# Optimization experiments

Hardware: AMD Instinct MI355X
Metric: run time of the kernel (lower is better)

Reference implementation:

```python
import jax, jax.numpy as jnp
import numpy as np

N_NODES = 50000
N_EDGES = 800000
DIM = 256
DEPTH = 4
N_REL = 4
EPS = 1e-5


def setup_inputs() -> dict:
    key = jax.random.key(0)
    ks = jax.random.split(key, 8)
    scale = 1.0 / np.sqrt(DIM)
    return {
        "node_embedding": jax.random.normal(ks[0], (N_NODES, DIM), jnp.float32),
        "weights": jax.random.normal(ks[1], (DEPTH, N_REL, DIM, DIM), jnp.float32) * scale,
        "roots": jax.random.normal(ks[2], (DEPTH, DIM, DIM), jnp.float32) * scale,
        "biases": jax.random.normal(ks[3], (DEPTH, DIM), jnp.float32) * 0.01,
        "ln_gamma": jnp.ones((DEPTH, DIM), jnp.float32),
        "ln_beta": jnp.zeros((DEPTH, DIM), jnp.float32),
        "edge_index": jax.random.randint(ks[4], (2, N_EDGES), 0, N_NODES, jnp.int32),
        "edge_type": jax.random.randint(ks[5], (N_EDGES,), 0, N_REL, jnp.int32),
    }


def _rgcn_layer(X, W, root, bias, gamma, beta, src, dst, etype, inv_deg):
    # RGCNConv with aggr='mean': per-relation transform, then per-relation mean
    # over incoming edges at the target node, summed across relations.
    h = jnp.einsum('ni,rio->rno', X, W)            # [R, N, D]
    msg = h[etype, src] * inv_deg[:, None]         # [E, D] gather + per-relation 1/deg
    agg = jax.ops.segment_sum(msg, dst, num_segments=X.shape[0])  # [N, D]
    out = agg + X @ root + bias
    # LayerNorm
    mu = jnp.mean(out, axis=-1, keepdims=True)
    var = jnp.mean(jnp.square(out - mu), axis=-1, keepdims=True)
    out = (out - mu) * jax.lax.rsqrt(var + EPS) * gamma + beta
    out = jax.nn.elu(out)
    return out + X  # residual connection (dropout p=0 -> identity)


def reference(node_embedding, weights, roots, biases, ln_gamma, ln_beta, edge_index, edge_type):
    src, dst = edge_index[0], edge_index[1]
    # per-(node, relation) in-degree for the relation-wise mean aggregation
    cnt = jnp.zeros((node_embedding.shape[0], N_REL), node_embedding.dtype)
    cnt = cnt.at[dst, edge_type].add(1.0)
    inv_deg = 1.0 / jnp.maximum(cnt[dst, edge_type], 1.0)  # [E]
    X = node_embedding
    for l in range(DEPTH):
        X = _rgcn_layer(X, weights[l], roots[l], biases[l], ln_gamma[l], ln_beta[l],
                        src, dst, edge_type, inv_deg)
    return X
```

## Files before the change

### kernel.cpp

```cpp
#include <hip/hip_runtime.h>
#include <hip/hip_bf16.h>
#include <stdint.h>

#define NN 50000
#define NE 800000
#define DD 256
#define NL 4
#define NRL 4
#define KT 1280
#define KA 1024
#define NMT 782
#define MTB 131072
#define NTILE 40

typedef float f32x4 __attribute__((ext_vector_type(4)));
typedef __bf16 bf16x8 __attribute__((ext_vector_type(8)));
typedef __bf16 bf16x4 __attribute__((ext_vector_type(4)));
typedef unsigned short u16x4 __attribute__((ext_vector_type(4)));

static __device__ __forceinline__ unsigned short f2bf(float f) {
  __bf16 h = (__bf16)f;
  return __builtin_bit_cast(unsigned short, h);
}

static __device__ __forceinline__ u16x4 pk4(f32x4 v) {
  u16x4 o;
  o.x = f2bf(v.x); o.y = f2bf(v.y); o.z = f2bf(v.z); o.w = f2bf(v.w);
  return o;
}

static __device__ __forceinline__ void async16(const void* g, void* l) {
  __builtin_amdgcn_global_load_lds(
      (const __attribute__((address_space(1))) unsigned int*)g,
      (__attribute__((address_space(3))) unsigned int*)l, 16, 0, 0);
}


__global__ __launch_bounds__(256) void k_hist(const int* __restrict__ ei,
                                              const int* __restrict__ et,
                                              int* __restrict__ cntNR) {
  int e = blockIdx.x * 256 + threadIdx.x;
  if (e >= NE) return;
  int dst = ei[NE + e];
  int r = et[e];
  atomicAdd(&cntNR[dst * 4 + r], 1);
}

__global__ __launch_bounds__(256) void k_scan1(const int* __restrict__ cntNR,
                                               int* __restrict__ offs,
                                               int* __restrict__ bsum) {
  __shared__ int sd[256];
  const int t = threadIdx.x;
  const int n = blockIdx.x * 256 + t;
  int deg = 0;
  if (n < NN) {
    const int* c = cntNR + n * 4;
    deg = c[0] + c[1] + c[2] + c[3];
  }
  sd[t] = deg;
  __syncthreads();
  int val = deg;
  for (int d = 1; d < 256; d <<= 1) {
    int other = (t >= d) ? sd[t - d] : 0;
    __syncthreads();
    val += other;
    sd[t] = val;
    __syncthreads();
  }
  if (n < NN) offs[n] = val - deg;
  if (t == 255) bsum[blockIdx.x] = val;
}

__global__ __launch_bounds__(256) void k_scan2(const int* __restrict__ bsum,
                                               int* __restrict__ boff, int nb) {
  __shared__ int sd[256];
  const int t = threadIdx.x;
  int v = (t < nb) ? bsum[t] : 0;
  sd[t] = v;
  __syncthreads();
  int val = v;
  for (int d = 1; d < 256; d <<= 1) {
    int other = (t >= d) ? sd[t - d] : 0;
    __syncthreads();
    val += other;
    sd[t] = val;
    __syncthreads();
  }
  boff[t] = val - v;
}

__global__ __launch_bounds__(256) void k_scan3(int* __restrict__ offs,
                                               const int* __restrict__ boff,
                                               int* __restrict__ cursor) {
  int n = blockIdx.x * 256 + threadIdx.x;
  if (n < NN) {
    int o = offs[n] + boff[blockIdx.x];
    offs[n] = o;
    cursor[n] = o;
  }
  if (n == 0) offs[NN] = NE;
}

__global__ __launch_bounds__(256) void k_scatter(const int* __restrict__ ei,
                                                 const int* __restrict__ et,
                                                 int* __restrict__ cursor,
                                                 uint32_t* __restrict__ packed) {
  int e = blockIdx.x * 256 + threadIdx.x;
  if (e >= NE) return;
  int src = ei[e];
  int dst = ei[NE + e];
  int r = et[e];
  int pos = atomicAdd(&cursor[dst], 1);
  packed[pos] = (uint32_t)src | ((uint32_t)r << 16);
}

__global__ __launch_bounds__(256) void k_wconv(const float* __restrict__ weights,
                                               const float* __restrict__ roots,
                                               __hip_bfloat16* __restrict__ WbigT) {
  int idx = blockIdx.x * 256 + threadIdx.x;
  if (idx >= NL * DD * KT) return;
  int l = idx / 327680;
  int rem = idx - l * 327680;
  int kt = rem / 8192;
  int rem2 = rem - kt * 8192;
  int row = rem2 >> 5;
  int q = rem2 & 31;
  int s = q >> 3, e = q & 7;
  int k = kt * 32 + ((s ^ ((row >> 1) & 3)) << 3) + e;
  float v;
  if (k < KA) {
    int r = k >> 8, i = k & 255;
    v = weights[(((size_t)(l * NRL + r) * DD) + i) * DD + row];
  } else {
    int i = k - KA;
    v = roots[((size_t)l * DD + i) * DD + row];
  }
  WbigT[idx] = __float2bfloat16(v);
}

__global__ __launch_bounds__(256) void k_cast(const float* __restrict__ X,
                                              __hip_bfloat16* __restrict__ Xbf) {
  int i = blockIdx.x * 256 + threadIdx.x;
  if (i >= NN * 64) return;
  const f32x4* Xv = (const f32x4*)X;
  ((u16x4*)Xbf)[i] = pk4(Xv[i]);
}


__global__ __launch_bounds__(256) void k_agg(const __hip_bfloat16* __restrict__ Xbf,
                                             const uint32_t* __restrict__ packed,
                                             const int* __restrict__ offs,
                                             const int* __restrict__ cntNR,
                                             __hip_bfloat16* __restrict__ Abig) {
  const int wid = (blockIdx.x * 256 + threadIdx.x) >> 6;
  const int lane = threadIdx.x & 63;
  if (wid >= NN) return;
  const int beg = offs[wid];
  const int end = offs[wid + 1];
  const bf16x4* __restrict__ Xv = (const bf16x4*)Xbf;

  f32x4 a0 = {0.f, 0.f, 0.f, 0.f}, a1 = a0, a2 = a0, a3 = a0;

  for (int e = beg; e < end; e += 8) {
    uint32_t pv[8];
    bf16x4 vv[8];
#pragma unroll
    for (int i = 0; i < 8; ++i) {
      int ee = e + i;
      ee = (ee < end) ? ee : (end - 1);
      pv[i] = packed[ee];
    }
#pragma unroll
    for (int i = 0; i < 8; ++i) {
      vv[i] = Xv[(int)(pv[i] & 0xFFFFu) * 64 + lane];
    }
    const int nv = end - e;
#pragma unroll
    for (int i = 0; i < 8; ++i) {
      if (i < nv) {
        int r = (int)(pv[i] >> 16);
        f32x4 v = {(float)vv[i][0], (float)vv[i][1], (float)vv[i][2], (float)vv[i][3]};
        if (r == 0) a0 += v;
        else if (r == 1) a1 += v;
        else if (r == 2) a2 += v;
        else a3 += v;
      }
    }
  }

  const int* c = cntNR + wid * 4;
  int c0 = c[0], c1 = c[1], c2 = c[2], c3 = c[3];
  float s0 = 1.0f / (float)(c0 > 1 ? c0 : 1);
  float s1 = 1.0f / (float)(c1 > 1 ? c1 : 1);
  float s2 = 1.0f / (float)(c2 > 1 ? c2 : 1);
  float s3 = 1.0f / (float)(c3 > 1 ? c3 : 1);

  {
    const int row = wid & 63;
    const int fsw = (row >> 1) & 3;
    char* Ab = (char*)Abig + (size_t)(wid >> 6) * MTB + (size_t)(lane >> 3) * 4096 +
               row * 64 + ((((lane >> 1) & 3) ^ fsw) << 4) + (lane & 1) * 8;
    *(u16x4*)(Ab + 0 * 32768) = pk4(a0 * s0);
    *(u16x4*)(Ab + 1 * 32768) = pk4(a1 * s1);
    *(u16x4*)(Ab + 2 * 32768) = pk4(a2 * s2);
    *(u16x4*)(Ab + 3 * 32768) = pk4(a3 * s3);
  }
}


#define GBUF 20480
#define EPAD 260

__global__ __launch_bounds__(256, 2) void k_gemm(const __hip_bfloat16* __restrict__ A,
                                                 const __hip_bfloat16* __restrict__ Xbf_in,
                                                 const __hip_bfloat16* __restrict__ Bt,
                                                 const float* __restrict__ bias,
                                                 const float* __restrict__ gamma,
                                                 const float* __restrict__ beta,
                                                 const float* __restrict__ Xin,
                                                 float* __restrict__ Xout,
                                                 __hip_bfloat16* __restrict__ Xbf_out) {
  __shared__ __align__(16) char sLDS[4 * GBUF];
  float(*LDSf)[EPAD] = (float(*)[EPAD])sLDS;
  float(*sRed)[4] = (float(*)[4])(sLDS + 69632);

  const int tid = threadIdx.x;
  const int w = tid >> 6;
  const int lane = tid & 63;
  const int wm = w >> 1, wn = w & 1;
  const int quad = lane >> 4, l15 = lane & 15;
  const int mBase = blockIdx.x * 64;

  const int srow = lane >> 2;
  const int kc = (lane & 3) ^ ((srow >> 1) & 3);
  int am = mBase + w * 16 + srow;
  if (am >= NN) am = NN - 1;
  const char* agx = (const char*)Xbf_in + (size_t)am * (DD * 2) + kc * 16;

  const char* agp = (const char*)A + (size_t)blockIdx.x * MTB + w * 1024 + lane * 16;
  const char* bgp = (const char*)Bt + w * 4096 + lane * 16;

  char* const lA = sLDS + w * 1024;
  char* const lB = sLDS + 4096 + w * 4096;

  f32x4 acc[2][8];
#pragma unroll
  for (int i = 0; i < 2; ++i)
#pragma unroll
    for (int j = 0; j < 8; ++j) acc[i][j] = (f32x4){0.f, 0.f, 0.f, 0.f};

  const int aslot = (quad ^ ((l15 >> 1) & 3)) * 16;
  const char* const aBase = sLDS + (wm * 32 + l15) * 64 + aslot;
  const char* const bBase = sLDS + 4096 + (wn * 128 + l15) * 64 + aslot;

  auto STAGE = [&](int buf, int ts) {
    char* la = lA + buf * GBUF;
    char* lb = lB + buf * GBUF;
    if (ts < 32) {
      async16(agp + (size_t)ts * 4096, la);
    } else {
      async16(agx + (ts - 32) * 64, la);
    }
    const char* bt = bgp + (size_t)ts * 16384;
    async16(bt, lb);
    async16(bt + 1024, lb + 1024);
    async16(bt + 2048, lb + 2048);
    async16(bt + 3072, lb + 3072);
  };

  auto COMPUTE = [&](int buf) {
    const char* aAddr = aBase + buf * GBUF;
    const char* bAddr = bBase + buf * GBUF;
    bf16x8 a0 = *(const bf16x8*)(aAddr + 0 * 1024);
    bf16x8 a1 = *(const bf16x8*)(aAddr + 1 * 1024);
#pragma unroll
    for (int nt = 0; nt < 8; ++nt) {
      bf16x8 b = *(const bf16x8*)(bAddr + nt * 1024);
      acc[0][nt] = __builtin_amdgcn_mfma_f32_16x16x32_bf16(a0, b, acc[0][nt], 0, 0, 0);
      acc[1][nt] = __builtin_amdgcn_mfma_f32_16x16x32_bf16(a1, b, acc[1][nt], 0, 0, 0);
    }
  };

  STAGE(0, 0);
  STAGE(1, 1);
  int cb = 0, sb = 2;
  for (int t = 0; t < NTILE - 2; ++t) {
    STAGE(sb, t + 2);
    __builtin_amdgcn_sched_barrier(0);
    asm volatile("s_waitcnt vmcnt(10)" ::: "memory");
    __builtin_amdgcn_s_barrier();
    __builtin_amdgcn_sched_barrier(0);
    COMPUTE(cb);
    cb = (cb + 1) & 3;
    sb = (sb + 1) & 3;
  }
  asm volatile("s_waitcnt vmcnt(5)" ::: "memory");
  __builtin_amdgcn_s_barrier();
  __builtin_amdgcn_sched_barrier(0);
  COMPUTE(cb);
  cb = (cb + 1) & 3;
  asm volatile("s_waitcnt vmcnt(0)" ::: "memory");
  __builtin_amdgcn_s_barrier();
  __builtin_amdgcn_sched_barrier(0);
  COMPUTE(cb);

  __syncthreads();

  float bv[8], gv[8], bev[8];
#pragma unroll
  for (int nt = 0; nt < 8; ++nt) {
    int n = wn * 128 + nt * 16 + l15;
    bv[nt] = bias[n];
    gv[nt] = gamma[n];
    bev[nt] = beta[n];
  }

#pragma unroll
  for (int mt = 0; mt < 2; ++mt) {
#pragma unroll
    for (int reg = 0; reg < 4; ++reg) {
      float s = 0.f, q = 0.f;
#pragma unroll
      for (int nt = 0; nt < 8; ++nt) {
        float v = acc[mt][nt][reg] + bv[nt];
        acc[mt][nt][reg] = v;
        s += v;
        q += v * v;
      }
#pragma unroll
      for (int d = 1; d < 16; d <<= 1) {
        s += __shfl_xor(s, d, 64);
        q += __shfl_xor(q, d, 64);
      }
      if (l15 == 0) {
        int row = wm * 32 + mt * 16 + quad * 4 + reg;
        sRed[row][wn * 2] = s;
        sRed[row][wn * 2 + 1] = q;
      }
    }
  }
  __syncthreads();

#pragma unroll
  for (int mt = 0; mt < 2; ++mt) {
#pragma unroll
    for (int reg = 0; reg < 4; ++reg) {
      int row = wm * 32 + mt * 16 + quad * 4 + reg;
      float ts = sRed[row][0] + sRed[row][2];
      float tq = sRed[row][1] + sRed[row][3];
      float mean = ts * (1.0f / 256.0f);
      float var = tq * (1.0f / 256.0f) - mean * mean;
      float rstd = rsqrtf(var + 1e-5f);
#pragma unroll
      for (int nt = 0; nt < 8; ++nt) {
        float v = (acc[mt][nt][reg] - mean) * rstd * gv[nt] + bev[nt];
        v = v > 0.0f ? v : (__expf(v) - 1.0f);
        LDSf[row][wn * 128 + nt * 16 + l15] = v;
      }
    }
  }
  __syncthreads();

#pragma unroll
  for (int rr = 0; rr < 16; ++rr) {
    const int row = w * 16 + rr;
    const int m = mBase + row;
    if (m < NN) {
      f32x4 v = *(const f32x4*)&LDSf[row][lane * 4];
      f32x4 xi = __builtin_nontemporal_load((const f32x4*)(Xin + (size_t)m * 256 + lane * 4));
      f32x4 res = v + xi;
      __builtin_nontemporal_store(res, (f32x4*)(Xout + (size_t)m * 256 + lane * 4));
      *(u16x4*)(Xbf_out + (size_t)m * 256 + lane * 4) = pk4(res);
    }
  }
}


extern "C" void kernel_launch(void* const* d_in, const int* in_sizes, int n_in,
                              void* d_out, int out_size, void* d_ws, size_t ws_size,
                              hipStream_t stream) {
  const float* X0 = (const float*)d_in[0];
  const float* weights = (const float*)d_in[1];
  const float* roots = (const float*)d_in[2];
  const float* biases = (const float*)d_in[3];
  const float* ln_g = (const float*)d_in[4];
  const float* ln_b = (const float*)d_in[5];
  const int* eidx = (const int*)d_in[6];
  const int* etyp = (const int*)d_in[7];
  float* out = (float*)d_out;

  char* ws = (char*)d_ws;
  size_t off = 0;
  auto alloc = [&](size_t bytes) -> char* {
    char* p = ws + off;
    off = (off + bytes + 255) & ~(size_t)255;
    return p;
  };
  __hip_bfloat16* Abig = (__hip_bfloat16*)alloc((size_t)NMT * MTB);
  __hip_bfloat16* WbigT = (__hip_bfloat16*)alloc((size_t)NL * DD * KT * 2);
  float* Xb0 = (float*)alloc((size_t)NN * DD * 4);
  float* Xb1 = (float*)alloc((size_t)NN * DD * 4);
  __hip_bfloat16* Xbf0 = (__hip_bfloat16*)alloc((size_t)NN * DD * 2);
  __hip_bfloat16* Xbf1 = (__hip_bfloat16*)alloc((size_t)NN * DD * 2);
  int* cntNR = (int*)alloc((size_t)NN * 4 * 4);
  int* offs = (int*)alloc((size_t)(NN + 1) * 4);
  int* cursor = (int*)alloc((size_t)NN * 4);
  uint32_t* packed = (uint32_t*)alloc((size_t)NE * 4);
  int* bsum = (int*)alloc(256 * 4);
  int* boff = (int*)alloc(256 * 4);
  (void)ws_size; (void)in_sizes; (void)n_in; (void)out_size;

  (void)hipMemsetAsync(cntNR, 0, (size_t)NN * 16, stream);
  (void)hipMemsetAsync((char*)Abig + (size_t)(NMT - 1) * MTB, 0, MTB, stream);
  k_hist<<<(NE + 255) / 256, 256, 0, stream>>>(eidx, etyp, cntNR);
  const int NB = (NN + 255) / 256;
  k_scan1<<<NB, 256, 0, stream>>>(cntNR, offs, bsum);
  k_scan2<<<1, 256, 0, stream>>>(bsum, boff, NB);
  k_scan3<<<NB, 256, 0, stream>>>(offs, boff, cursor);
  k_scatter<<<(NE + 255) / 256, 256, 0, stream>>>(eidx, etyp, cursor, packed);
  k_wconv<<<(NL * DD * KT + 255) / 256, 256, 0, stream>>>(weights, roots, WbigT);
  k_cast<<<(NN * 64 + 255) / 256, 256, 0, stream>>>(X0, Xbf0);

  const float* Xin = X0;
  for (int l = 0; l < NL; ++l) {
    float* Xout = (l == NL - 1) ? out : ((l & 1) ? Xb1 : Xb0);
    const __hip_bfloat16* Xbin = (l & 1) ? Xbf1 : Xbf0;
    __hip_bfloat16* Xbout = (l & 1) ? Xbf0 : Xbf1;
    k_agg<<<(NN * 64 + 255) / 256, 256, 0, stream>>>(Xbin, packed, offs, cntNR, Abig);
    k_gemm<<<(NN + 63) / 64, 256, 0, stream>>>(Abig, Xbin,
                                               WbigT + (size_t)l * DD * KT,
                                               biases + (size_t)l * DD,
                                               ln_g + (size_t)l * DD,
                                               ln_b + (size_t)l * DD, Xin, Xout, Xbout);
    Xin = Xout;
  }
}
```

Before: 800.7 us.

## Fuse edge aggregation into GEMM kernel with relation-sorted CSR

Removes the separate aggregation kernel and its global A buffer. Each GEMM block now gathers neighbor features per relation straight into LDS, then runs the MFMA K-tiles for that relation while weight tiles stream in with a 3-buffer async pipeline. Edges are now sorted by (dst, relation) using per-relation cursors, so the relation branch disappears from the inner loop. This cuts the global write and read of the aggregated activations, but the irregular gathers now sit inside the GEMM blocks, with less latency hiding and per-relation barriers.

```diff
diff --git a/kernel.cpp b/kernel.cpp
--- a/kernel.cpp
+++ b/kernel.cpp
@@ -10,7 +10,6 @@
 #define KT 1280
 #define KA 1024
 #define NMT 782
-#define MTB 131072
 #define NTILE 40
 
 typedef float f32x4 __attribute__((ext_vector_type(4)));
@@ -91,27 +90,32 @@
 
 __global__ __launch_bounds__(256) void k_scan3(int* __restrict__ offs,
                                                const int* __restrict__ boff,
-                                               int* __restrict__ cursor) {
+                                               const int* __restrict__ cntNR,
+                                               int* __restrict__ cursor4) {
   int n = blockIdx.x * 256 + threadIdx.x;
   if (n < NN) {
     int o = offs[n] + boff[blockIdx.x];
     offs[n] = o;
-    cursor[n] = o;
+    const int4 c = *(const int4*)(cntNR + n * 4);
+    cursor4[n * 4 + 0] = o;
+    cursor4[n * 4 + 1] = o + c.x;
+    cursor4[n * 4 + 2] = o + c.x + c.y;
+    cursor4[n * 4 + 3] = o + c.x + c.y + c.z;
   }
   if (n == 0) offs[NN] = NE;
 }
 
 __global__ __launch_bounds__(256) void k_scatter(const int* __restrict__ ei,
                                                  const int* __restrict__ et,
-                                                 int* __restrict__ cursor,
+                                                 int* __restrict__ cursor4,
                                                  uint32_t* __restrict__ packed) {
   int e = blockIdx.x * 256 + threadIdx.x;
   if (e >= NE) return;
   int src = ei[e];
   int dst = ei[NE + e];
   int r = et[e];
-  int pos = atomicAdd(&cursor[dst], 1);
-  packed[pos] = (uint32_t)src | ((uint32_t)r << 16);
+  int pos = atomicAdd(&cursor4[dst * 4 + r], 1);
+  packed[pos] = (uint32_t)src;
 }
 
 __global__ __launch_bounds__(256) void k_wconv(const float* __restrict__ weights,
@@ -147,72 +151,10 @@
 }
 
 
-__global__ __launch_bounds__(256) void k_agg(const __hip_bfloat16* __restrict__ Xbf,
-                                             const uint32_t* __restrict__ packed,
-                                             const int* __restrict__ offs,
-                                             const int* __restrict__ cntNR,
-                                             __hip_bfloat16* __restrict__ Abig) {
-  const int wid = (blockIdx.x * 256 + threadIdx.x) >> 6;
-  const int lane = threadIdx.x & 63;
-  if (wid >= NN) return;
-  const int beg = offs[wid];
-  const int end = offs[wid + 1];
-  const bf16x4* __restrict__ Xv = (const bf16x4*)Xbf;
-
-  f32x4 a0 = {0.f, 0.f, 0.f, 0.f}, a1 = a0, a2 = a0, a3 = a0;
-
-  for (int e = beg; e < end; e += 8) {
-    uint32_t pv[8];
-    bf16x4 vv[8];
-#pragma unroll
-    for (int i = 0; i < 8; ++i) {
-      int ee = e + i;
-      ee = (ee < end) ? ee : (end - 1);
-      pv[i] = packed[ee];
-    }
-#pragma unroll
-    for (int i = 0; i < 8; ++i) {
-      vv[i] = Xv[(int)(pv[i] & 0xFFFFu) * 64 + lane];
-    }
-    const int nv = end - e;
-#pragma unroll
-    for (int i = 0; i < 8; ++i) {
-      if (i < nv) {
-        int r = (int)(pv[i] >> 16);
-        f32x4 v = {(float)vv[i][0], (float)vv[i][1], (float)vv[i][2], (float)vv[i][3]};
-        if (r == 0) a0 += v;
-        else if (r == 1) a1 += v;
-        else if (r == 2) a2 += v;
-        else a3 += v;
-      }
-    }
-  }
-
-  const int* c = cntNR + wid * 4;
-  int c0 = c[0], c1 = c[1], c2 = c[2], c3 = c[3];
-  float s0 = 1.0f / (float)(c0 > 1 ? c0 : 1);
-  float s1 = 1.0f / (float)(c1 > 1 ? c1 : 1);
-  float s2 = 1.0f / (float)(c2 > 1 ? c2 : 1);
-  float s3 = 1.0f / (float)(c3 > 1 ? c3 : 1);
-
-  {
-    const int row = wid & 63;
-    const int fsw = (row >> 1) & 3;
-    char* Ab = (char*)Abig + (size_t)(wid >> 6) * MTB + (size_t)(lane >> 3) * 4096 +
-               row * 64 + ((((lane >> 1) & 3) ^ fsw) << 4) + (lane & 1) * 8;
-    *(u16x4*)(Ab + 0 * 32768) = pk4(a0 * s0);
-    *(u16x4*)(Ab + 1 * 32768) = pk4(a1 * s1);
-    *(u16x4*)(Ab + 2 * 32768) = pk4(a2 * s2);
-    *(u16x4*)(Ab + 3 * 32768) = pk4(a3 * s3);
-  }
-}
-
-
-#define GBUF 20480
-#define EPAD 260
-
-__global__ __launch_bounds__(256, 2) void k_gemm(const __hip_bfloat16* __restrict__ A,
-                                                 const __hip_bfloat16* __restrict__ Xbf_in,
+__global__ __launch_bounds__(256, 2) void k_rgcn(const __hip_bfloat16* __restrict__ Xbf_in,
+                                                 const uint32_t* __restrict__ packed,
+                                                 const int* __restrict__ offs,
+                                                 const int* __restrict__ cntNR,
                                                  const __hip_bfloat16* __restrict__ Bt,
                                                  const float* __restrict__ bias,
                                                  const float* __restrict__ gamma,
@@ -220,7 +162,8 @@
                                                  const float* __restrict__ Xin,
                                                  float* __restrict__ Xout,
                                                  __hip_bfloat16* __restrict__ Xbf_out) {
-  __shared__ __align__(16) char sLDS[4 * GBUF];
+  __shared__ __align__(16) char sLDS[81920];
+#define EPAD 260
   float(*LDSf)[EPAD] = (float(*)[EPAD])sLDS;
   float(*sRed)[4] = (float(*)[4])(sLDS + 69632);
 
@@ -231,36 +174,22 @@
   const int quad = lane >> 4, l15 = lane & 15;
   const int mBase = blockIdx.x * 64;
 
-  const int srow = lane >> 2;
-  const int kc = (lane & 3) ^ ((srow >> 1) & 3);
-  int am = mBase + w * 16 + srow;
-  if (am >= NN) am = NN - 1;
-  const char* agx = (const char*)Xbf_in + (size_t)am * (DD * 2) + kc * 16;
-
-  const char* agp = (const char*)A + (size_t)blockIdx.x * MTB + w * 1024 + lane * 16;
   const char* bgp = (const char*)Bt + w * 4096 + lane * 16;
-
-  char* const lA = sLDS + w * 1024;
-  char* const lB = sLDS + 4096 + w * 4096;
-
-  f32x4 acc[2][8];
-#pragma unroll
-  for (int i = 0; i < 2; ++i)
-#pragma unroll
-    for (int j = 0; j < 8; ++j) acc[i][j] = (f32x4){0.f, 0.f, 0.f, 0.f};
 
   const int aslot = (quad ^ ((l15 >> 1) & 3)) * 16;
   const char* const aBase = sLDS + (wm * 32 + l15) * 64 + aslot;
-  const char* const bBase = sLDS + 4096 + (wn * 128 + l15) * 64 + aslot;
-
-  auto STAGE = [&](int buf, int ts) {
-    char* la = lA + buf * GBUF;
-    char* lb = lB + buf * GBUF;
-    if (ts < 32) {
-      async16(agp + (size_t)ts * 4096, la);
-    } else {
-      async16(agx + (ts - 32) * 64, la);
-    }
+  const char* const bBase = sLDS + 32768 + (wn * 128 + l15) * 64 + aslot;
+
+  const bf16x4* __restrict__ Xv = (const bf16x4*)Xbf_in;
+
+  f32x4 acc[2][8];
+#pragma unroll
+  for (int i = 0; i < 2; ++i)
+#pragma unroll
+    for (int j = 0; j < 8; ++j) acc[i][j] = (f32x4){0.f, 0.f, 0.f, 0.f};
+
+  auto STAGE_B = [&](int buf, int ts) {
+    char* lb = sLDS + 32768 + buf * 16384 + w * 4096;
     const char* bt = bgp + (size_t)ts * 16384;
     async16(bt, lb);
     async16(bt + 1024, lb + 1024);
@@ -268,11 +197,11 @@
     async16(bt + 3072, lb + 3072);
   };
 
-  auto COMPUTE = [&](int buf) {
-    const char* aAddr = aBase + buf * GBUF;
-    const char* bAddr = bBase + buf * GBUF;
-    bf16x8 a0 = *(const bf16x8*)(aAddr + 0 * 1024);
-    bf16x8 a1 = *(const bf16x8*)(aAddr + 1 * 1024);
+  auto COMPUTE = [&](int t8, int bb) {
+    const char* aAddr = aBase + t8 * 4096;
+    const char* bAddr = bBase + bb * 16384;
+    bf16x8 a0 = *(const bf16x8*)(aAddr);
+    bf16x8 a1 = *(const bf16x8*)(aAddr + 1024);
 #pragma unroll
     for (int nt = 0; nt < 8; ++nt) {
       bf16x8 b = *(const bf16x8*)(bAddr + nt * 1024);
@@ -281,29 +210,91 @@
     }
   };
 
-  STAGE(0, 0);
-  STAGE(1, 1);
-  int cb = 0, sb = 2;
-  for (int t = 0; t < NTILE - 2; ++t) {
-    STAGE(sb, t + 2);
-    __builtin_amdgcn_sched_barrier(0);
-    asm volatile("s_waitcnt vmcnt(10)" ::: "memory");
-    __builtin_amdgcn_s_barrier();
-    __builtin_amdgcn_sched_barrier(0);
-    COMPUTE(cb);
-    cb = (cb + 1) & 3;
-    sb = (sb + 1) & 3;
-  }
-  asm volatile("s_waitcnt vmcnt(5)" ::: "memory");
-  __builtin_amdgcn_s_barrier();
-  __builtin_amdgcn_sched_barrier(0);
-  COMPUTE(cb);
-  cb = (cb + 1) & 3;
-  asm volatile("s_waitcnt vmcnt(0)" ::: "memory");
-  __builtin_amdgcn_s_barrier();
-  __builtin_amdgcn_sched_barrier(0);
-  COMPUTE(cb);
-
+  auto AGG = [&](int r) {
+    for (int rr = 0; rr < 16; ++rr) {
+      const int row = w * 16 + rr;
+      int n = mBase + row;
+      if (n >= NN) n = NN - 1;
+      const int4 c = *(const int4*)(cntNR + n * 4);
+      int beg = offs[n];
+      int cr;
+      if (r == 0) { cr = c.x; }
+      else if (r == 1) { beg += c.x; cr = c.y; }
+      else if (r == 2) { beg += c.x + c.y; cr = c.z; }
+      else { beg += c.x + c.y + c.z; cr = c.w; }
+      const int end = beg + cr;
+      f32x4 a = {0.f, 0.f, 0.f, 0.f};
+      for (int e = beg; e < end; e += 4) {
+        uint32_t pv[4];
+        bf16x4 vv[4];
+#pragma unroll
+        for (int i = 0; i < 4; ++i) {
+          int ee = e + i;
+          ee = (ee < end) ? ee : (end - 1);
+          pv[i] = packed[ee];
+        }
+#pragma unroll
+        for (int i = 0; i < 4; ++i) vv[i] = Xv[(int)pv[i] * 64 + lane];
+        const int nv = end - e;
+#pragma unroll
+        for (int i = 0; i < 4; ++i) {
+          if (i < nv) {
+            a.x += (float)vv[i][0];
+            a.y += (float)vv[i][1];
+            a.z += (float)vv[i][2];
+            a.w += (float)vv[i][3];
+          }
+        }
+      }
+      const float s = 1.0f / (float)(cr > 1 ? cr : 1);
+      const int fsw = (row >> 1) & 3;
+      char* dst = sLDS + (size_t)(lane >> 3) * 4096 + row * 64 +
+                  ((((lane >> 1) & 3) ^ fsw) << 4) + (lane & 1) * 8;
+      *(u16x4*)dst = pk4(a * s);
+    }
+  };
+
+  auto ROOT = [&]() {
+    for (int rr = 0; rr < 16; ++rr) {
+      const int row = w * 16 + rr;
+      int n = mBase + row;
+      if (n >= NN) n = NN - 1;
+      bf16x4 v = Xv[n * 64 + lane];
+      const int fsw = (row >> 1) & 3;
+      char* dst = sLDS + (size_t)(lane >> 3) * 4096 + row * 64 +
+                  ((((lane >> 1) & 3) ^ fsw) << 4) + (lane & 1) * 8;
+      *(bf16x4*)dst = v;
+    }
+  };
+
+  STAGE_B(0, 0);
+  STAGE_B(1, 1);
+
+  int bb = 0;
+  for (int r = 0; r < 5; ++r) {
+    if (r) {
+      __builtin_amdgcn_sched_barrier(0);
+      __builtin_amdgcn_s_barrier();
+      __builtin_amdgcn_sched_barrier(0);
+    }
+    if (r < 4) AGG(r); else ROOT();
+    __syncthreads();
+#pragma unroll
+    for (int t8 = 0; t8 < 8; ++t8) {
+      const int t = r * 8 + t8;
+      if (r == 4 && t8 == 7) {
+        asm volatile("s_waitcnt vmcnt(0)" ::: "memory");
+      } else {
+        asm volatile("s_waitcnt vmcnt(4)" ::: "memory");
+      }
+      __builtin_amdgcn_s_barrier();
+      __builtin_amdgcn_sched_barrier(0);
+      if (t + 2 < 40) STAGE_B((bb + 2 == 3) ? 0 : ((bb + 2 == 4) ? 1 : bb + 2), t + 2);
+      __builtin_amdgcn_sched_barrier(0);
+      COMPUTE(t8, bb);
+      bb = (bb == 2) ? 0 : bb + 1;
+    }
+  }
   __syncthreads();
 
   float bv[8], gv[8], bev[8];
@@ -396,7 +387,6 @@
     off = (off + bytes + 255) & ~(size_t)255;
     return p;
   };
-  __hip_bfloat16* Abig = (__hip_bfloat16*)alloc((size_t)NMT * MTB);
   __hip_bfloat16* WbigT = (__hip_bfloat16*)alloc((size_t)NL * DD * KT * 2);
   float* Xb0 = (float*)alloc((size_t)NN * DD * 4);
   float* Xb1 = (float*)alloc((size_t)NN * DD * 4);
@@ -404,20 +394,19 @@
   __hip_bfloat16* Xbf1 = (__hip_bfloat16*)alloc((size_t)NN * DD * 2);
   int* cntNR = (int*)alloc((size_t)NN * 4 * 4);
   int* offs = (int*)alloc((size_t)(NN + 1) * 4);
-  int* cursor = (int*)alloc((size_t)NN * 4);
+  int* cursor4 = (int*)alloc((size_t)NN * 4 * 4);
   uint32_t* packed = (uint32_t*)alloc((size_t)NE * 4);
   int* bsum = (int*)alloc(256 * 4);
   int* boff = (int*)alloc(256 * 4);
   (void)ws_size; (void)in_sizes; (void)n_in; (void)out_size;
 
   (void)hipMemsetAsync(cntNR, 0, (size_t)NN * 16, stream);
-  (void)hipMemsetAsync((char*)Abig + (size_t)(NMT - 1) * MTB, 0, MTB, stream);
   k_hist<<<(NE + 255) / 256, 256, 0, stream>>>(eidx, etyp, cntNR);
   const int NB = (NN + 255) / 256;
   k_scan1<<<NB, 256, 0, stream>>>(cntNR, offs, bsum);
   k_scan2<<<1, 256, 0, stream>>>(bsum, boff, NB);
-  k_scan3<<<NB, 256, 0, stream>>>(offs, boff, cursor);
-  k_scatter<<<(NE + 255) / 256, 256, 0, stream>>>(eidx, etyp, cursor, packed);
+  k_scan3<<<NB, 256, 0, stream>>>(offs, boff, cntNR, cursor4);
+  k_scatter<<<(NE + 255) / 256, 256, 0, stream>>>(eidx, etyp, cursor4, packed);
   k_wconv<<<(NL * DD * KT + 255) / 256, 256, 0, stream>>>(weights, roots, WbigT);
   k_cast<<<(NN * 64 + 255) / 256, 256, 0, stream>>>(X0, Xbf0);
 
@@ -426,12 +415,11 @@
     float* Xout = (l == NL - 1) ? out : ((l & 1) ? Xb1 : Xb0);
     const __hip_bfloat16* Xbin = (l & 1) ? Xbf1 : Xbf0;
     __hip_bfloat16* Xbout = (l & 1) ? Xbf0 : Xbf1;
-    k_agg<<<(NN * 64 + 255) / 256, 256, 0, stream>>>(Xbin, packed, offs, cntNR, Abig);
-    k_gemm<<<(NN + 63) / 64, 256, 0, stream>>>(Abig, Xbin,
-                                               WbigT + (size_t)l * DD * KT,
-                                               biases + (size_t)l * DD,
-                                               ln_g + (size_t)l * DD,
-                                               ln_b + (size_t)l * DD, Xin, Xout, Xbout);
+    k_rgcn<<<NMT, 256, 0, stream>>>(Xbin, packed, offs, cntNR,
+                                    WbigT + (size_t)l * DD * KT,
+                                    biases + (size_t)l * DD,
+                                    ln_g + (size_t)l * DD,
+                                    ln_b + (size_t)l * DD, Xin, Xout, Xbout);
     Xin = Xout;
   }
 }
```

After: 1.427 ms. +78.2%, slower.

## Bucket CSR edges by relation and gather 16-byte rows with half-wave split

Applied to the files above, without the earlier changes.

The CSR build now keeps a cursor per (node, relation), so each node's edges come out grouped by relation and the relation bits no longer need to be packed into the edge word. The aggregation kernel then walks each relation bucket separately, so the per-edge relation branching goes away. Each half-wave gathers a different edge with 16-byte bf16x8 loads, and the two halves are combined with a cross-lane shuffle. Results are written as 16-byte nontemporal stores, at the cost of more serial loop passes per node (four buckets) and masked wasted loads when bucket sizes are not multiples of four.

```diff
diff --git a/kernel.cpp b/kernel.cpp
--- a/kernel.cpp
+++ b/kernel.cpp
@@ -17,6 +17,7 @@
 typedef __bf16 bf16x8 __attribute__((ext_vector_type(8)));
 typedef __bf16 bf16x4 __attribute__((ext_vector_type(4)));
 typedef unsigned short u16x4 __attribute__((ext_vector_type(4)));
+typedef unsigned short u16x8 __attribute__((ext_vector_type(8)));
 
 static __device__ __forceinline__ unsigned short f2bf(float f) {
   __bf16 h = (__bf16)f;
@@ -26,6 +27,13 @@
 static __device__ __forceinline__ u16x4 pk4(f32x4 v) {
   u16x4 o;
   o.x = f2bf(v.x); o.y = f2bf(v.y); o.z = f2bf(v.z); o.w = f2bf(v.w);
+  return o;
+}
+
+static __device__ __forceinline__ u16x8 pk8(f32x4 lo, f32x4 hi) {
+  u16x8 o;
+  o[0] = f2bf(lo.x); o[1] = f2bf(lo.y); o[2] = f2bf(lo.z); o[3] = f2bf(lo.w);
+  o[4] = f2bf(hi.x); o[5] = f2bf(hi.y); o[6] = f2bf(hi.z); o[7] = f2bf(hi.w);
   return o;
 }
 
@@ -91,27 +99,32 @@
 
 __global__ __launch_bounds__(256) void k_scan3(int* __restrict__ offs,
                                                const int* __restrict__ boff,
-                                               int* __restrict__ cursor) {
+                                               const int* __restrict__ cntNR,
+                                               int* __restrict__ cursor4) {
   int n = blockIdx.x * 256 + threadIdx.x;
   if (n < NN) {
     int o = offs[n] + boff[blockIdx.x];
     offs[n] = o;
-    cursor[n] = o;
+    const int4 c = *(const int4*)(cntNR + n * 4);
+    cursor4[n * 4 + 0] = o;
+    cursor4[n * 4 + 1] = o + c.x;
+    cursor4[n * 4 + 2] = o + c.x + c.y;
+    cursor4[n * 4 + 3] = o + c.x + c.y + c.z;
   }
   if (n == 0) offs[NN] = NE;
 }
 
 __global__ __launch_bounds__(256) void k_scatter(const int* __restrict__ ei,
                                                  const int* __restrict__ et,
-                                                 int* __restrict__ cursor,
+                                                 int* __restrict__ cursor4,
                                                  uint32_t* __restrict__ packed) {
   int e = blockIdx.x * 256 + threadIdx.x;
   if (e >= NE) return;
   int src = ei[e];
   int dst = ei[NE + e];
   int r = et[e];
-  int pos = atomicAdd(&cursor[dst], 1);
-  packed[pos] = (uint32_t)src | ((uint32_t)r << 16);
+  int pos = atomicAdd(&cursor4[dst * 4 + r], 1);
+  packed[pos] = (uint32_t)src;
 }
 
 __global__ __launch_bounds__(256) void k_wconv(const float* __restrict__ weights,
@@ -155,55 +168,57 @@
   const int wid = (blockIdx.x * 256 + threadIdx.x) >> 6;
   const int lane = threadIdx.x & 63;
   if (wid >= NN) return;
-  const int beg = offs[wid];
-  const int end = offs[wid + 1];
-  const bf16x4* __restrict__ Xv = (const bf16x4*)Xbf;
-
-  f32x4 a0 = {0.f, 0.f, 0.f, 0.f}, a1 = a0, a2 = a0, a3 = a0;
-
-  for (int e = beg; e < end; e += 8) {
-    uint32_t pv[8];
-    bf16x4 vv[8];
-#pragma unroll
-    for (int i = 0; i < 8; ++i) {
-      int ee = e + i;
-      ee = (ee < end) ? ee : (end - 1);
-      pv[i] = packed[ee];
-    }
-#pragma unroll
-    for (int i = 0; i < 8; ++i) {
-      vv[i] = Xv[(int)(pv[i] & 0xFFFFu) * 64 + lane];
-    }
-    const int nv = end - e;
-#pragma unroll
-    for (int i = 0; i < 8; ++i) {
-      if (i < nv) {
-        int r = (int)(pv[i] >> 16);
-        f32x4 v = {(float)vv[i][0], (float)vv[i][1], (float)vv[i][2], (float)vv[i][3]};
-        if (r == 0) a0 += v;
-        else if (r == 1) a1 += v;
-        else if (r == 2) a2 += v;
-        else a3 += v;
-      }
-    }
-  }
-
-  const int* c = cntNR + wid * 4;
-  int c0 = c[0], c1 = c[1], c2 = c[2], c3 = c[3];
-  float s0 = 1.0f / (float)(c0 > 1 ? c0 : 1);
-  float s1 = 1.0f / (float)(c1 > 1 ? c1 : 1);
-  float s2 = 1.0f / (float)(c2 > 1 ? c2 : 1);
-  float s3 = 1.0f / (float)(c3 > 1 ? c3 : 1);
-
-  {
-    const int row = wid & 63;
-    const int fsw = (row >> 1) & 3;
-    char* Ab = (char*)Abig + (size_t)(wid >> 6) * MTB + (size_t)(lane >> 3) * 4096 +
-               row * 64 + ((((lane >> 1) & 3) ^ fsw) << 4) + (lane & 1) * 8;
-    *(u16x4*)(Ab + 0 * 32768) = pk4(a0 * s0);
-    *(u16x4*)(Ab + 1 * 32768) = pk4(a1 * s1);
-    *(u16x4*)(Ab + 2 * 32768) = pk4(a2 * s2);
-    *(u16x4*)(Ab + 3 * 32768) = pk4(a3 * s3);
+  const int g = lane >> 5;
+  const int j = lane & 31;
+  const bf16x8* __restrict__ Xv8 = (const bf16x8*)Xbf;
+
+  const int4 c = *(const int4*)(cntNR + wid * 4);
+  const int crArr[4] = {c.x, c.y, c.z, c.w};
+  int s = offs[wid];
+
+  const int row = wid & 63;
+  const int fsw = (row >> 1) & 3;
+  char* const Ab = (char*)Abig + (size_t)(wid >> 6) * MTB + row * 64 +
+                   (((j & 3) ^ fsw) << 4);
+
+#pragma unroll
+  for (int r = 0; r < 4; ++r) {
+    const int cr = crArr[r];
+    const int end = s + cr;
+    f32x4 aLo = {0.f, 0.f, 0.f, 0.f}, aHi = aLo;
+    for (int e = s; e < end; e += 4) {
+      int e0 = e + g;
+      int e1 = e + 2 + g;
+      const float m0 = (e0 < end) ? 1.f : 0.f;
+      const float m1 = (e1 < end) ? 1.f : 0.f;
+      e0 = (e0 < end) ? e0 : end - 1;
+      e1 = (e1 < end) ? e1 : end - 1;
+      const uint32_t p0 = packed[e0];
+      const uint32_t p1 = packed[e1];
+      const bf16x8 x0 = Xv8[(int)p0 * 32 + j];
+      const bf16x8 x1 = Xv8[(int)p1 * 32 + j];
+#pragma unroll
+      for (int k2 = 0; k2 < 4; ++k2) {
+        aLo[k2] += (float)x0[k2] * m0;
+        aHi[k2] += (float)x0[4 + k2] * m0;
+      }
+#pragma unroll
+      for (int k2 = 0; k2 < 4; ++k2) {
+        aLo[k2] += (float)x1[k2] * m1;
+        aHi[k2] += (float)x1[4 + k2] * m1;
+      }
+    }
+#pragma unroll
+    for (int k2 = 0; k2 < 4; ++k2) {
+      aLo[k2] += __shfl_xor(aLo[k2], 32, 64);
+      aHi[k2] += __shfl_xor(aHi[k2], 32, 64);
+    }
+    const float sc = 1.0f / (float)(cr > 1 ? cr : 1);
+    if (g == 0) {
+      __builtin_nontemporal_store(pk8(aLo * sc, aHi * sc),
+                                  (u16x8*)(Ab + (size_t)(r * 8 + (j >> 2)) * 4096));
+    }
+    s = end;
   }
 }
 
@@ -404,7 +419,7 @@
   __hip_bfloat16* Xbf1 = (__hip_bfloat16*)alloc((size_t)NN * DD * 2);
   int* cntNR = (int*)alloc((size_t)NN * 4 * 4);
   int* offs = (int*)alloc((size_t)(NN + 1) * 4);
-  int* cursor = (int*)alloc((size_t)NN * 4);
+  int* cursor4 = (int*)alloc((size_t)NN * 4 * 4);
   uint32_t* packed = (uint32_t*)alloc((size_t)NE * 4);
   int* bsum = (int*)alloc(256 * 4);
   int* boff = (int*)alloc(256 * 4);
@@ -416,8 +431,8 @@
   const int NB = (NN + 255) / 256;
   k_scan1<<<NB, 256, 0, stream>>>(cntNR, offs, bsum);
   k_scan2<<<1, 256, 0, stream>>>(bsum, boff, NB);
-  k_scan3<<<NB, 256, 0, stream>>>(offs, boff, cursor);
-  k_scatter<<<(NE + 255) / 256, 256, 0, stream>>>(eidx, etyp, cursor, packed);
+  k_scan3<<<NB, 256, 0, stream>>>(offs, boff, cntNR, cursor4);
+  k_scatter<<<(NE + 255) / 256, 256, 0, stream>>>(eidx, etyp, cursor4, packed);
   k_wconv<<<(NL * DD * KT + 255) / 256, 256, 0, stream>>>(weights, roots, WbigT);
   k_cast<<<(NN * 64 + 255) / 256, 256, 0, stream>>>(X0, Xbf0);
 
```

Result: no change. 812.1 us (+1.4%).
